# Optimization experiments

Measured on AMD Instinct MI355X. Metric: run time of the kernel, lower is better.

## Reference

```python
import jax, jax.numpy as jnp
import numpy as np

B, S, T, E, H = 16, 96, 50, 128, 128
D2 = 2 * H
V = 32000
NGRAM = 2
ALPHA = 0.25


def _lstm(x, Wih, Whh, b, reverse=False):
    # x: [N, T, E] -> outputs [N, T, H], final h, c (PyTorch gate order i,f,g,o)
    xt = jnp.swapaxes(x, 0, 1)
    if reverse:
        xt = xt[::-1]
    n = x.shape[0]
    h = Whh.shape[1]
    init = (jnp.zeros((n, h), x.dtype), jnp.zeros((n, h), x.dtype))

    def step(carry, xin):
        hprev, cprev = carry
        g = xin @ Wih.T + hprev @ Whh.T + b
        i, f, gg, o = jnp.split(g, 4, axis=-1)
        c = jax.nn.sigmoid(f) * cprev + jax.nn.sigmoid(i) * jnp.tanh(gg)
        hnew = jax.nn.sigmoid(o) * jnp.tanh(c)
        return (hnew, c), hnew

    (hT, cT), outs = jax.lax.scan(step, init, xt)
    if reverse:
        outs = outs[::-1]
    return jnp.swapaxes(outs, 0, 1), hT, cT


def _gru(x, h, Wi, Wh, bi, bh):
    # PyTorch GRUCell, gate order r,z,n
    gi = x @ Wi.T + bi
    gh = h @ Wh.T + bh
    ir, iz, inn = jnp.split(gi, 3, axis=-1)
    hr, hz, hn = jnp.split(gh, 3, axis=-1)
    r = jax.nn.sigmoid(ir + hr)
    z = jax.nn.sigmoid(iz + hz)
    n = jnp.tanh(inn + r * hn)
    return (1.0 - z) * n + z * h


def _norm_scale(x):
    # (||x|| + alpha) / (||x|| + 1), detached as in the original
    v = jnp.linalg.norm(x, axis=1)
    return jax.lax.stop_gradient(((v + ALPHA) / (v + 1.0))[:, None])


def setup_inputs() -> dict:
    key = jax.random.key(0)
    ks = jax.random.split(key, 30)
    rn = lambda k, sh: jax.random.normal(k, sh, jnp.float32) * 0.05
    return {
        "enc_batch": jax.random.randint(ks[0], (B * S, T), 0, V),
        "struct_parent": jax.random.randint(ks[1], (B, S, S), 0, B * S + 1),
        "struct_child": jax.random.randint(ks[2], (B, S, S), 0, B * S + 1),
        "mask_emb": (jax.random.uniform(ks[3], (B, S, S, 1)) < 0.2).astype(jnp.float32),
        "emb_table": rn(ks[4], (V, E)),
        "Wih_f": rn(ks[5], (4 * H, E)), "Whh_f": rn(ks[6], (4 * H, H)), "b_f": rn(ks[7], (4 * H,)),
        "Wih_b": rn(ks[8], (4 * H, E)), "Whh_b": rn(ks[9], (4 * H, H)), "b_b": rn(ks[10], (4 * H,)),
        "Wc": rn(ks[11], (H, D2)), "bc": rn(ks[12], (H,)),
        "Whr": rn(ks[13], (H, D2)), "bhr": rn(ks[14], (H,)),
        "Wi_cp": rn(ks[15], (3 * D2, D2)), "Wh_cp": rn(ks[16], (3 * D2, D2)),
        "bi_cp": rn(ks[17], (3 * D2,)), "bh_cp": rn(ks[18], (3 * D2,)),
        "Wi_pc": rn(ks[19], (3 * D2, D2)), "Wh_pc": rn(ks[20], (3 * D2, D2)),
        "bi_pc": rn(ks[21], (3 * D2,)), "bh_pc": rn(ks[22], (3 * D2,)),
    }


def reference(enc_batch, struct_parent, struct_child, mask_emb, emb_table,
              Wih_f, Whh_f, b_f, Wih_b, Whh_b, b_b, Wc, bc, Whr, bhr,
              Wi_cp, Wh_cp, bi_cp, bh_cp, Wi_pc, Wh_pc, bi_pc, bh_pc):
    # Sentence encoder (bidirectional LSTM); dropout=0 -> identity
    emb = emb_table[enc_batch]                       # [B*S, T, E]
    _, hf, cf = _lstm(emb, Wih_f, Whh_f, b_f)
    _, hb, cb = _lstm(emb, Wih_b, Whh_b, b_b, reverse=True)
    c_red = jax.nn.relu(jnp.concatenate([cf, cb], 1) @ Wc.T + bc)
    h_red = jax.nn.relu(jnp.concatenate([hf, hb], 1) @ Whr.T + bhr)
    enc_states = jnp.concatenate([c_red, h_red], 1)  # [B*S, 2H]
    zero = jnp.zeros((1, D2), enc_states.dtype)
    hidden = jnp.concatenate([zero, enc_states], 0)  # [B*S+1, 2H]; row 0 = zero_emb

    # child -> parent message passing
    for _ in range(NGRAM):
        p = hidden[struct_parent].reshape(-1, D2)    # gather [B*S*S, 2H]
        c = hidden[struct_child].reshape(-1, D2)
        ch = _gru(c, p, Wi_cp, Wh_cp, bi_cp, bh_cp).reshape(B, S, S, D2)
        ch = (ch * mask_emb).sum(1).reshape(B * S, D2)
        ch = jnp.concatenate([zero, ch], 0)
        hidden = hidden + ch * _norm_scale(ch)

    # parent -> child message passing
    for _ in range(NGRAM):
        p = hidden[struct_parent].reshape(-1, D2)
        c = hidden[struct_child].reshape(-1, D2)
        ch = _gru(p, c, Wi_pc, Wh_pc, bi_pc, bh_pc).reshape(B, S, S, D2)
        ch = (ch * mask_emb).sum(2).reshape(B * S, D2)
        ch = jnp.concatenate([zero, ch], 0)
        hidden = hidden + ch * _norm_scale(ch)

    return hidden
```

## Files before the change

kernel.cpp:

```cpp
#include <hip/hip_runtime.h>

typedef unsigned short u16;
typedef __attribute__((ext_vector_type(8))) short bf8;
typedef __attribute__((ext_vector_type(4))) short s16x4;
typedef __attribute__((ext_vector_type(4))) float f32x4;
typedef __attribute__((ext_vector_type(4))) int   i32x4;

#define S_   96
#define T_   50
#define NSEQ 1536
#define NR   1537
#define XROW 530

__device__ __forceinline__ float bf2f(u16 u){ return __uint_as_float(((unsigned)u)<<16); }
__device__ __forceinline__ u16 f2bf(float f){
  unsigned u = __float_as_uint(f);
  u += 0x7fffu + ((u>>16)&1u);
  return (u16)(u>>16);
}
__device__ __forceinline__ float sigm(float x){
  return __builtin_amdgcn_rcpf(1.f + __expf(-x));
}
__device__ __forceinline__ float tanh_(float x){
  return 1.f - 2.f*__builtin_amdgcn_rcpf(__expf(2.f*x) + 1.f);
}

struct CvtArgs { const float* s[10]; u16* d[10]; };
__global__ __launch_bounds__(256) void cvt_kernel(CvtArgs a){
  int e = (blockIdx.x*256 + threadIdx.x)*4;
  if (e >= 1114112) return;
  int t, off;
  if (e < 262144){ t = e>>16; off = e & 65535; }
  else if (e < 327680){ int e2=e-262144; t = 4+(e2>>15); off = e2&32767; }
  else { int e3=e-327680; t = 6 + e3/196608; off = e3%196608; }
  int src = off;
  if (t < 4){
    int colp = off>>7, k = off&127;
    int orig = ((colp>>4)&3)*128 + ((colp>>6)<<4) + (colp&15);
    src = orig*128 + k;
  }
  f32x4 v = *reinterpret_cast<const f32x4*>(a.s[t]+src);
  s16x4 o;
  #pragma unroll
  for (int i=0;i<4;i++) o[i]=(short)f2bf(v[i]);
  *reinterpret_cast<s16x4*>(a.d[t]+off) = o;
}

__global__ __launch_bounds__(128) void build_lists(
    const int* __restrict__ par, const int* __restrict__ chi,
    const float* __restrict__ mask,
    int2* __restrict__ ent0, int* __restrict__ cnt0,
    int2* __restrict__ ent1, int* __restrict__ cnt1)
{
  const int rr = blockIdx.x;
  __shared__ int c0s, c1s;
  if (threadIdx.x==0){ c0s=0; c1s=0; }
  __syncthreads();
  const int l = threadIdx.x;
  if (l < S_){
    const int b = rr/S_, fx = rr%S_, base = b*S_*S_;
    int idx = base + l*S_ + fx;
    if (mask[idx] != 0.f){
      int p = atomicAdd(&c0s, 1);
      ent0[rr*S_ + p] = make_int2(chi[idx], par[idx]);
    }
    int jdx = base + fx*S_ + l;
    if (mask[jdx] != 0.f){
      int p = atomicAdd(&c1s, 1);
      ent1[rr*S_ + p] = make_int2(par[jdx], chi[jdx]);
    }
  }
  __syncthreads();
  if (threadIdx.x==0){ cnt0[rr]=c0s; cnt1[rr]=c1s; }
}

__global__ __launch_bounds__(512, 2) void lstm_kernel(
    const int* __restrict__ enc, const float* __restrict__ emb,
    const u16* __restrict__ WihF, const u16* __restrict__ WhhF, const float* __restrict__ bF,
    const u16* __restrict__ WihB, const u16* __restrict__ WhhB, const float* __restrict__ bB,
    u16* __restrict__ c_cat, u16* __restrict__ h_cat)
{
  __shared__ short xh[16*XROW];
  __shared__ int   toks[16*T_];

  const int tid  = threadIdx.x;
  const int wave = tid>>6;
  const int lane = tid&63;
  const int dir  = blockIdx.y;
  const int s0   = blockIdx.x*16;

  const u16* Wih = dir ? WihB : WihF;
  const u16* Whh = dir ? WhhB : WhhF;
  const float* bb = dir ? bB  : bF;

  for (int i=tid; i<16*T_; i+=512)
    toks[i] = enc[(s0 + i/T_)*T_ + (i%T_)];

  const int mL   = lane&15;
  const int quad = lane>>4;
  const int kb   = quad*8;

  bf8 Breg[4][8];
  float bias[4];
  #pragma unroll
  for (int n=0;n<4;n++){
    int colp = wave*64 + n*16 + mL;
    bias[n] = bb[n*128 + wave*16 + mL];
    #pragma unroll
    for (int ks=0;ks<8;ks++){
      int k = ks*32 + kb;
      const u16* p = (k<128) ? (Wih + colp*128 + k) : (Whh + colp*128 + (k-128));
      Breg[n][ks] = *reinterpret_cast<const bf8*>(p);
      asm volatile("" : "+v"(Breg[n][ks]));
    }
  }

  if (tid<256){
    int r = tid>>4, c = tid&15;
    *reinterpret_cast<i32x4*>(&xh[r*XROW + 256 + c*8]) = (i32x4){0,0,0,0};
  }

  const int srow = tid>>5, schunk = tid&31;
  float cst[4] = {0.f,0.f,0.f,0.f};
  float hst[4] = {0.f,0.f,0.f,0.f};

  __syncthreads();

  {
    int tok = toks[srow*T_ + (dir ? (T_-1) : 0)];
    f32x4 xv = *reinterpret_cast<const f32x4*>(emb + tok*128 + schunk*4);
    s16x4 xp;
    #pragma unroll
    for (int i=0;i<4;i++) xp[i]=(short)f2bf(xv[i]);
    *reinterpret_cast<s16x4*>(&xh[srow*XROW + schunk*4]) = xp;
  }
  f32x4 xv1, xv2;
  {
    int tok1 = toks[srow*T_ + (dir ? (T_-2) : 1)];
    xv1 = *reinterpret_cast<const f32x4*>(emb + tok1*128 + schunk*4);
    int tok2 = toks[srow*T_ + (dir ? (T_-3) : 2)];
    xv2 = *reinterpret_cast<const f32x4*>(emb + tok2*128 + schunk*4);
  }
  __syncthreads();

  for (int t=0;t<T_;t++){
    const int cb = t&1, nb2 = (t+1)&1;
    if (t+1 < T_){
      s16x4 xp;
      #pragma unroll
      for (int i=0;i<4;i++) xp[i]=(short)f2bf(xv1[i]);
      *reinterpret_cast<s16x4*>(&xh[srow*XROW + nb2*128 + schunk*4]) = xp;
    }
    xv1 = xv2;
    if (t+3 < T_){
      int tok = toks[srow*T_ + (dir ? (T_-4-t) : (t+3))];
      xv2 = *reinterpret_cast<const f32x4*>(emb + tok*128 + schunk*4);
    }

    f32x4 acc[4];
    #pragma unroll
    for (int i=0;i<4;i++) acc[i] = (f32x4){0.f,0.f,0.f,0.f};
    #pragma unroll
    for (int ks=0;ks<8;ks++){
      int k = ks*32 + kb;
      int off = (k<128) ? (cb*128 + k) : (256 + cb*128 + (k-128));
      bf8 a = *reinterpret_cast<const bf8*>(&xh[mL*XROW + off]);
      #pragma unroll
      for (int n=0;n<4;n++)
        acc[n] = __builtin_amdgcn_mfma_f32_16x16x32_bf16(a, Breg[n][ks], acc[n], 0,0,0);
    }

    #pragma unroll
    for (int i=0;i<4;i++){
      float gi_ = acc[0][i]+bias[0];
      float gf_ = acc[1][i]+bias[1];
      float gg_ = acc[2][i]+bias[2];
      float go_ = acc[3][i]+bias[3];
      float c = sigm(gf_)*cst[i] + sigm(gi_)*tanh_(gg_);
      float h = sigm(go_)*tanh_(c);
      cst[i]=c; hst[i]=h;
      xh[(quad*4+i)*XROW + 256 + nb2*128 + wave*16 + mL] = (short)f2bf(h);
    }
    __syncthreads();
  }

  {
    const int ch = wave*16 + mL;
    #pragma unroll
    for (int i=0;i<4;i++){
      int gs = s0 + quad*4 + i;
      c_cat[gs*256 + dir*128 + ch] = f2bf(cst[i]);
      h_cat[gs*256 + dir*128 + ch] = f2bf(hst[i]);
    }
  }
}

__global__ __launch_bounds__(256) void reduce_kernel(
    const u16* __restrict__ c_cat, const u16* __restrict__ h_cat,
    const u16* __restrict__ Wc, const float* __restrict__ bc,
    const u16* __restrict__ Whr, const float* __restrict__ bhr,
    float* __restrict__ hidf, u16* __restrict__ hidb)
{
  const int tid=threadIdx.x, wave=tid>>6, lane=tid&63;
  const int mL=lane&15, quad=lane>>4, kb=quad*8;
  const int m0 = blockIdx.x*64;
  const u16* A    = (wave<2) ? c_cat : h_cat;
  const u16* W    = (wave<2) ? Wc  : Whr;
  const float* bv = (wave<2) ? bc  : bhr;
  const int nb    = (wave&1)*64;
  const int obase = (wave<2) ? 0 : 128;

  f32x4 acc[4][4];
  #pragma unroll
  for (int mt=0;mt<4;mt++)
    #pragma unroll
    for (int nt=0;nt<4;nt++) acc[mt][nt] = (f32x4){0.f,0.f,0.f,0.f};

  #pragma unroll
  for (int ks=0;ks<8;ks++){
    int k = ks*32 + kb;
    bf8 bfr[4];
    #pragma unroll
    for (int nt=0;nt<4;nt++)
      bfr[nt] = *reinterpret_cast<const bf8*>(W + (nb+nt*16+mL)*256 + k);
    #pragma unroll
    for (int mt=0;mt<4;mt++){
      bf8 a = *reinterpret_cast<const bf8*>(A + (m0+mt*16+mL)*256 + k);
      #pragma unroll
      for (int nt=0;nt<4;nt++)
        acc[mt][nt] = __builtin_amdgcn_mfma_f32_16x16x32_bf16(a, bfr[nt], acc[mt][nt], 0,0,0);
    }
  }
  const int row0 = quad*4;
  float biasv[4];
  #pragma unroll
  for (int nt=0;nt<4;nt++) biasv[nt] = bv[nb+nt*16+mL];
  #pragma unroll
  for (int mt=0;mt<4;mt++){
    #pragma unroll
    for (int nt=0;nt<4;nt++){
      int col = obase + nb + nt*16 + mL;
      #pragma unroll
      for (int i=0;i<4;i++){
        int r = m0 + mt*16 + row0 + i;
        float v = fmaxf(acc[mt][nt][i] + biasv[nt], 0.f);
        hidf[(r+1)*256 + col] = v;
        hidb[(r+1)*256 + col] = f2bf(v);
      }
    }
  }
  if (blockIdx.x==0 && tid<64){
    #pragma unroll
    for (int j=0;j<4;j++){ hidf[tid*4+j] = 0.f; hidb[tid*4+j] = 0; }
  }
}

__global__ __launch_bounds__(256) void gates_gemm_kernel(
    const u16* __restrict__ hidb,
    const u16* __restrict__ Wi, const u16* __restrict__ Wh,
    const float* __restrict__ bi, const float* __restrict__ bh,
    u16* __restrict__ gi, u16* __restrict__ gh)
{
  const int tid=threadIdx.x, wave=tid>>6, lane=tid&63;
  const int mL=lane&15, quad=lane>>4, kb=quad*8;
  const int m0 = blockIdx.x*32;
  const int n0 = blockIdx.y*256 + wave*64;
  const bool isI = (n0 < 768);
  const u16* W    = isI ? Wi : Wh;
  const float* bv = isI ? bi : bh;
  u16* out        = isI ? gi : gh;
  const int nbc   = isI ? n0 : (n0-768);

  int arow[2];
  #pragma unroll
  for (int mt=0;mt<2;mt++) arow[mt] = min(m0+mt*16+mL, NR-1);

  f32x4 acc[2][4];
  #pragma unroll
  for (int mt=0;mt<2;mt++)
    #pragma unroll
    for (int nt=0;nt<4;nt++) acc[mt][nt] = (f32x4){0.f,0.f,0.f,0.f};

  #pragma unroll
  for (int ks=0;ks<8;ks++){
    int k = ks*32 + kb;
    bf8 bfr[4];
    #pragma unroll
    for (int nt=0;nt<4;nt++)
      bfr[nt] = *reinterpret_cast<const bf8*>(W + (nbc+nt*16+mL)*256 + k);
    #pragma unroll
    for (int mt=0;mt<2;mt++){
      bf8 a = *reinterpret_cast<const bf8*>(hidb + arow[mt]*256 + k);
      #pragma unroll
      for (int nt=0;nt<4;nt++)
        acc[mt][nt] = __builtin_amdgcn_mfma_f32_16x16x32_bf16(a, bfr[nt], acc[mt][nt], 0,0,0);
    }
  }
  const int row0 = quad*4;
  float biasv[4];
  #pragma unroll
  for (int nt=0;nt<4;nt++) biasv[nt] = bv[nbc+nt*16+mL];
  #pragma unroll
  for (int mt=0;mt<2;mt++){
    #pragma unroll
    for (int nt=0;nt<4;nt++){
      #pragma unroll
      for (int i=0;i<4;i++){
        int r = m0 + mt*16 + row0 + i;
        if (r < NR)
          out[r*768 + nbc + nt*16 + mL] = f2bf(acc[mt][nt][i] + biasv[nt]);
      }
    }
  }
}

__global__ __launch_bounds__(512) void pair_kernel(
    const u16* __restrict__ gi, const u16* __restrict__ gh,
    const float* __restrict__ hin,
    float* __restrict__ hout, u16* __restrict__ bout, float* __restrict__ dout,
    const int2* __restrict__ ent, const int* __restrict__ cnt)
{
  const int r = blockIdx.x;
  const int tid = threadIdx.x, wave = tid>>6, lane = tid&63;
  __shared__ float part[8][260];
  __shared__ float ssum[4];
  if (r==0){
    if (tid<256){
      hout[tid]=0.f; bout[tid]=0;
      if (dout) dout[tid]=0.f;
    }
    return;
  }
  const int rr = r-1;
  const int n  = cnt[rr];
  const int2* e = ent + rr*S_;
  const int ch0 = lane*4;

  float a0=0.f, a1=0.f, a2=0.f, a3=0.f;
  for (int k=wave; k<n; k+=8){
    int2 pr = e[k];
    const u16* gx = gi + pr.x*768 + ch0;
    const u16* gy = gh + pr.y*768 + ch0;
    s16x4 vi0 = *reinterpret_cast<const s16x4*>(gx);
    s16x4 vi1 = *reinterpret_cast<const s16x4*>(gx+256);
    s16x4 vi2 = *reinterpret_cast<const s16x4*>(gx+512);
    s16x4 vh0 = *reinterpret_cast<const s16x4*>(gy);
    s16x4 vh1 = *reinterpret_cast<const s16x4*>(gy+256);
    s16x4 vh2 = *reinterpret_cast<const s16x4*>(gy+512);
    f32x4 hv  = *reinterpret_cast<const f32x4*>(hin + pr.y*256 + ch0);
    float o[4];
    #pragma unroll
    for (int i=0;i<4;i++){
      float rg = sigm(bf2f((u16)vi0[i]) + bf2f((u16)vh0[i]));
      float zg = sigm(bf2f((u16)vi1[i]) + bf2f((u16)vh1[i]));
      float ng = tanh_(bf2f((u16)vi2[i]) + rg*bf2f((u16)vh2[i]));
      o[i] = (1.f-zg)*ng + zg*hv[i];
    }
    a0 += o[0]; a1 += o[1]; a2 += o[2]; a3 += o[3];
  }
  *reinterpret_cast<f32x4*>(&part[wave][ch0]) = (f32x4){a0,a1,a2,a3};
  __syncthreads();

  if (tid < 256){
    float tot = part[0][tid] + part[1][tid] + part[2][tid] + part[3][tid]
              + part[4][tid] + part[5][tid] + part[6][tid] + part[7][tid];
    part[0][tid] = tot;
    float sq = tot*tot;
    #pragma unroll
    for (int off=32; off>0; off>>=1) sq += __shfl_xor(sq, off, 64);
    if (lane==0) ssum[wave] = sq;
  }
  __syncthreads();
  if (tid < 256){
    float tot = part[0][tid];
    float v  = sqrtf(ssum[0]+ssum[1]+ssum[2]+ssum[3]);
    float sc = (v + 0.25f)*__builtin_amdgcn_rcpf(v + 1.f);
    float nv = hin[r*256 + tid] + tot*sc;
    hout[r*256 + tid] = nv;
    bout[r*256 + tid] = f2bf(nv);
    if (dout) dout[r*256 + tid] = nv;
  }
}

extern "C" void kernel_launch(void* const* d_in, const int* in_sizes, int n_in,
                              void* d_out, int out_size, void* d_ws, size_t ws_size,
                              hipStream_t stream)
{
  const int*   enc  = (const int*)  d_in[0];
  const int*   spar = (const int*)  d_in[1];
  const int*   schi = (const int*)  d_in[2];
  const float* mask = (const float*)d_in[3];
  const float* emb  = (const float*)d_in[4];
  const float* WihF = (const float*)d_in[5];
  const float* WhhF = (const float*)d_in[6];
  const float* bF   = (const float*)d_in[7];
  const float* WihB = (const float*)d_in[8];
  const float* WhhB = (const float*)d_in[9];
  const float* bB   = (const float*)d_in[10];
  const float* Wc   = (const float*)d_in[11];
  const float* bc   = (const float*)d_in[12];
  const float* Whr  = (const float*)d_in[13];
  const float* bhr  = (const float*)d_in[14];
  const float* WiCP = (const float*)d_in[15];
  const float* WhCP = (const float*)d_in[16];
  const float* biCP = (const float*)d_in[17];
  const float* bhCP = (const float*)d_in[18];
  const float* WiPC = (const float*)d_in[19];
  const float* WhPC = (const float*)d_in[20];
  const float* biPC = (const float*)d_in[21];
  const float* bhPC = (const float*)d_in[22];

  char* ws = (char*)d_ws;
  u16*   c_cat = (u16*)  (ws + 0);
  u16*   h_cat = (u16*)  (ws + 786432);
  float* hf0   = (float*)(ws + 1572864);
  float* hf1   = (float*)(ws + 3146752);
  u16*   hb    = (u16*)  (ws + 4720640);
  u16*   gi    = (u16*)  (ws + 5507584);
  u16*   gh    = (u16*)  (ws + 7868416);
  u16*   wbf   = (u16*)  (ws + 10229248);
  int2*  ent0  = (int2*) (ws + 12457472);
  int2*  ent1  = (int2*) (ws + 13637120);
  int*   cnt0  = (int*)  (ws + 14816768);
  int*   cnt1  = (int*)  (ws + 14822912);
  float* out   = (float*)d_out;

  u16* bWihF = wbf + 0;
  u16* bWhhF = wbf + 65536;
  u16* bWihB = wbf + 131072;
  u16* bWhhB = wbf + 196608;
  u16* bWc   = wbf + 262144;
  u16* bWhr  = wbf + 294912;
  u16* bWiCP = wbf + 327680;
  u16* bWhCP = wbf + 524288;
  u16* bWiPC = wbf + 720896;
  u16* bWhPC = wbf + 917504;

  CvtArgs ca;
  ca.s[0]=WihF; ca.s[1]=WhhF; ca.s[2]=WihB; ca.s[3]=WhhB;
  ca.s[4]=Wc;   ca.s[5]=Whr;
  ca.s[6]=WiCP; ca.s[7]=WhCP; ca.s[8]=WiPC; ca.s[9]=WhPC;
  ca.d[0]=bWihF; ca.d[1]=bWhhF; ca.d[2]=bWihB; ca.d[3]=bWhhB;
  ca.d[4]=bWc;   ca.d[5]=bWhr;
  ca.d[6]=bWiCP; ca.d[7]=bWhCP; ca.d[8]=bWiPC; ca.d[9]=bWhPC;
  cvt_kernel<<<dim3(1088), dim3(256), 0, stream>>>(ca);
  build_lists<<<dim3(NSEQ), dim3(128), 0, stream>>>(spar, schi, mask, ent0, cnt0, ent1, cnt1);

  lstm_kernel<<<dim3(96,2), dim3(512), 0, stream>>>(
      enc, emb, bWihF,bWhhF,bF, bWihB,bWhhB,bB, c_cat, h_cat);
  reduce_kernel<<<dim3(24), dim3(256), 0, stream>>>(
      c_cat,h_cat, bWc,bc,bWhr,bhr, hf0,hb);

  float* hfb[2] = {hf0,hf1};
  int cur = 0;
  for (int it=0; it<4; it++){
    const u16* Wi   = (it<2)?bWiCP:bWiPC;
    const u16* Wh   = (it<2)?bWhCP:bWhPC;
    const float* bi = (it<2)?biCP:biPC;
    const float* bh = (it<2)?bhCP:bhPC;
    int nxt = cur^1;
    gates_gemm_kernel<<<dim3(49,6), dim3(256), 0, stream>>>(
        hb, Wi,Wh,bi,bh, gi,gh);
    pair_kernel<<<dim3(NR), dim3(512), 0, stream>>>(
        gi,gh, hfb[cur], hfb[nxt], hb,
        (it==3)?out:(float*)nullptr,
        (it<2)?ent0:ent1, (it<2)?cnt0:cnt1);
    cur = nxt;
  }
}
```

Baseline: 333.8 us.

## Transpose LSTM MFMA operands for vectorized h stores and merge prep kernels

Swaps the MFMA A/B operands in the LSTM step so each lane holds four consecutive gate columns for one sequence. The new hidden state can then go to LDS as a single 8-byte store, and the final c/h go to global memory as vector writes. Bias is loaded as a float4 to match, the LDS row stride drops from 530 to 520, and the full __syncthreads is replaced by an lgkmcnt wait plus s_barrier. It also merges the weight-conversion and list-building kernels into one launch, trading a launch for mixed block roles and possible LDS bank-conflict changes.

After: 325.9 us. 2.4% less time.

```diff
diff --git a/kernel.cpp b/kernel.cpp
--- a/kernel.cpp
+++ b/kernel.cpp
@@ -10,7 +10,7 @@
 #define T_   50
 #define NSEQ 1536
 #define NR   1537
-#define XROW 530
+#define XROW 520
 
 __device__ __forceinline__ float bf2f(u16 u){ return __uint_as_float(((unsigned)u)<<16); }
 __device__ __forceinline__ u16 f2bf(float f){
@@ -24,54 +24,57 @@
 __device__ __forceinline__ float tanh_(float x){
   return 1.f - 2.f*__builtin_amdgcn_rcpf(__expf(2.f*x) + 1.f);
 }
+__device__ __forceinline__ void bar_lds(){
+  asm volatile("s_waitcnt lgkmcnt(0)\n\ts_barrier" ::: "memory");
+}
 
 struct CvtArgs { const float* s[10]; u16* d[10]; };
-__global__ __launch_bounds__(256) void cvt_kernel(CvtArgs a){
-  int e = (blockIdx.x*256 + threadIdx.x)*4;
-  if (e >= 1114112) return;
-  int t, off;
-  if (e < 262144){ t = e>>16; off = e & 65535; }
-  else if (e < 327680){ int e2=e-262144; t = 4+(e2>>15); off = e2&32767; }
-  else { int e3=e-327680; t = 6 + e3/196608; off = e3%196608; }
-  int src = off;
-  if (t < 4){
-    int colp = off>>7, k = off&127;
-    int orig = ((colp>>4)&3)*128 + ((colp>>6)<<4) + (colp&15);
-    src = orig*128 + k;
-  }
-  f32x4 v = *reinterpret_cast<const f32x4*>(a.s[t]+src);
-  s16x4 o;
-  #pragma unroll
-  for (int i=0;i<4;i++) o[i]=(short)f2bf(v[i]);
-  *reinterpret_cast<s16x4*>(a.d[t]+off) = o;
-}
-
-__global__ __launch_bounds__(128) void build_lists(
+__global__ __launch_bounds__(256) void prep_kernel(CvtArgs a,
     const int* __restrict__ par, const int* __restrict__ chi,
     const float* __restrict__ mask,
     int2* __restrict__ ent0, int* __restrict__ cnt0,
     int2* __restrict__ ent1, int* __restrict__ cnt1)
 {
-  const int rr = blockIdx.x;
-  __shared__ int c0s, c1s;
-  if (threadIdx.x==0){ c0s=0; c1s=0; }
-  __syncthreads();
-  const int l = threadIdx.x;
-  if (l < S_){
-    const int b = rr/S_, fx = rr%S_, base = b*S_*S_;
-    int idx = base + l*S_ + fx;
-    if (mask[idx] != 0.f){
-      int p = atomicAdd(&c0s, 1);
-      ent0[rr*S_ + p] = make_int2(chi[idx], par[idx]);
-    }
-    int jdx = base + fx*S_ + l;
-    if (mask[jdx] != 0.f){
-      int p = atomicAdd(&c1s, 1);
-      ent1[rr*S_ + p] = make_int2(par[jdx], chi[jdx]);
-    }
-  }
-  __syncthreads();
-  if (threadIdx.x==0){ cnt0[rr]=c0s; cnt1[rr]=c1s; }
+  if (blockIdx.x < 1088){
+    int e = (blockIdx.x*256 + threadIdx.x)*4;
+    if (e >= 1114112) return;
+    int t, off;
+    if (e < 262144){ t = e>>16; off = e & 65535; }
+    else if (e < 327680){ int e2=e-262144; t = 4+(e2>>15); off = e2&32767; }
+    else { int e3=e-327680; t = 6 + e3/196608; off = e3%196608; }
+    int src = off;
+    if (t < 4){
+      int colp = off>>7, k = off&127;
+      int orig = ((colp>>4)&3)*128 + ((colp>>6)<<4) + (colp&15);
+      src = orig*128 + k;
+    }
+    f32x4 v = *reinterpret_cast<const f32x4*>(a.s[t]+src);
+    s16x4 o;
+    #pragma unroll
+    for (int i=0;i<4;i++) o[i]=(short)f2bf(v[i]);
+    *reinterpret_cast<s16x4*>(a.d[t]+off) = o;
+  } else {
+    const int rr = blockIdx.x - 1088;
+    __shared__ int c0s, c1s;
+    if (threadIdx.x==0){ c0s=0; c1s=0; }
+    __syncthreads();
+    const int l = threadIdx.x;
+    if (l < S_){
+      const int b = rr/S_, fx = rr%S_, base = b*S_*S_;
+      int idx = base + l*S_ + fx;
+      if (mask[idx] != 0.f){
+        int p = atomicAdd(&c0s, 1);
+        ent0[rr*S_ + p] = make_int2(chi[idx], par[idx]);
+      }
+      int jdx = base + fx*S_ + l;
+      if (mask[jdx] != 0.f){
+        int p = atomicAdd(&c1s, 1);
+        ent1[rr*S_ + p] = make_int2(par[jdx], chi[jdx]);
+      }
+    }
+    __syncthreads();
+    if (threadIdx.x==0){ cnt0[rr]=c0s; cnt1[rr]=c1s; }
+  }
 }
 
 __global__ __launch_bounds__(512, 2) void lstm_kernel(
@@ -101,11 +104,11 @@
   const int kb   = quad*8;
 
   bf8 Breg[4][8];
-  float bias[4];
+  f32x4 bias4[4];
   #pragma unroll
   for (int n=0;n<4;n++){
     int colp = wave*64 + n*16 + mL;
-    bias[n] = bb[n*128 + wave*16 + mL];
+    bias4[n] = *reinterpret_cast<const f32x4*>(bb + n*128 + wave*16 + quad*4);
     #pragma unroll
     for (int ks=0;ks<8;ks++){
       int k = ks*32 + kb;
@@ -164,34 +167,36 @@
     for (int ks=0;ks<8;ks++){
       int k = ks*32 + kb;
       int off = (k<128) ? (cb*128 + k) : (256 + cb*128 + (k-128));
-      bf8 a = *reinterpret_cast<const bf8*>(&xh[mL*XROW + off]);
+      bf8 b = *reinterpret_cast<const bf8*>(&xh[mL*XROW + off]);
       #pragma unroll
       for (int n=0;n<4;n++)
-        acc[n] = __builtin_amdgcn_mfma_f32_16x16x32_bf16(a, Breg[n][ks], acc[n], 0,0,0);
-    }
-
+        acc[n] = __builtin_amdgcn_mfma_f32_16x16x32_bf16(Breg[n][ks], b, acc[n], 0,0,0);
+    }
+
+    s16x4 hp;
     #pragma unroll
     for (int i=0;i<4;i++){
-      float gi_ = acc[0][i]+bias[0];
-      float gf_ = acc[1][i]+bias[1];
-      float gg_ = acc[2][i]+bias[2];
-      float go_ = acc[3][i]+bias[3];
+      float gi_ = acc[0][i]+bias4[0][i];
+      float gf_ = acc[1][i]+bias4[1][i];
+      float gg_ = acc[2][i]+bias4[2][i];
+      float go_ = acc[3][i]+bias4[3][i];
       float c = sigm(gf_)*cst[i] + sigm(gi_)*tanh_(gg_);
       float h = sigm(go_)*tanh_(c);
       cst[i]=c; hst[i]=h;
-      xh[(quad*4+i)*XROW + 256 + nb2*128 + wave*16 + mL] = (short)f2bf(h);
-    }
-    __syncthreads();
+      hp[i] = (short)f2bf(h);
+    }
+    *reinterpret_cast<s16x4*>(&xh[mL*XROW + 256 + nb2*128 + wave*16 + quad*4]) = hp;
+    bar_lds();
   }
 
   {
-    const int ch = wave*16 + mL;
-    #pragma unroll
-    for (int i=0;i<4;i++){
-      int gs = s0 + quad*4 + i;
-      c_cat[gs*256 + dir*128 + ch] = f2bf(cst[i]);
-      h_cat[gs*256 + dir*128 + ch] = f2bf(hst[i]);
-    }
+    const int ch = wave*16 + quad*4;
+    const int gs = s0 + mL;
+    s16x4 cp_, hp_;
+    #pragma unroll
+    for (int i=0;i<4;i++){ cp_[i]=(short)f2bf(cst[i]); hp_[i]=(short)f2bf(hst[i]); }
+    *reinterpret_cast<s16x4*>(c_cat + gs*256 + dir*128 + ch) = cp_;
+    *reinterpret_cast<s16x4*>(h_cat + gs*256 + dir*128 + ch) = hp_;
   }
 }
 
@@ -443,8 +448,8 @@
   ca.d[0]=bWihF; ca.d[1]=bWhhF; ca.d[2]=bWihB; ca.d[3]=bWhhB;
   ca.d[4]=bWc;   ca.d[5]=bWhr;
   ca.d[6]=bWiCP; ca.d[7]=bWhCP; ca.d[8]=bWiPC; ca.d[9]=bWhPC;
-  cvt_kernel<<<dim3(1088), dim3(256), 0, stream>>>(ca);
-  build_lists<<<dim3(NSEQ), dim3(128), 0, stream>>>(spar, schi, mask, ent0, cnt0, ent1, cnt1);
+  prep_kernel<<<dim3(1088+NSEQ), dim3(256), 0, stream>>>(
+      ca, spar, schi, mask, ent0, cnt0, ent1, cnt1);
 
   lstm_kernel<<<dim3(96,2), dim3(512), 0, stream>>>(
       enc, emb, bWihF,bWhhF,bF, bWihB,bWhhB,bB, c_cat, h_cat);
```
